# Optimization experiments

Hardware: AMD Instinct MI355X
Metric: run time of the kernel (lower is better)

The kernel has to match this reference:

```python
import jax, jax.numpy as jnp
import numpy as np

D_MODEL = 1024
N_HEADS = 16
D_K = D_MODEL // N_HEADS
B, S = 4, 2048
NEG = -1e9

def setup_inputs() -> dict:
    key = jax.random.key(0)
    ks = jax.random.split(key, 6)
    scale = 1.0 / np.sqrt(D_MODEL)
    x = jax.random.normal(ks[0], (B, S, D_MODEL), dtype=jnp.float32)
    mask = jnp.ones((B, S), dtype=jnp.int32)
    Wq = jax.random.normal(ks[1], (D_MODEL, D_MODEL), dtype=jnp.float32) * scale
    Wk = jax.random.normal(ks[2], (D_MODEL, D_MODEL), dtype=jnp.float32) * scale
    Wv = jax.random.normal(ks[3], (D_MODEL, D_MODEL), dtype=jnp.float32) * scale
    Wo = jax.random.normal(ks[4], (D_MODEL, D_MODEL), dtype=jnp.float32) * scale
    bo = jnp.zeros((D_MODEL,), dtype=jnp.float32)
    return {"x": x, "mask": mask, "Wq": Wq, "Wk": Wk, "Wv": Wv, "Wo": Wo, "bo": bo}

def reference(x, mask, Wq, Wk, Wv, Wo, bo):
    B_, S_ = x.shape[0], x.shape[1]
    # torch nn.Linear: y = x @ W.T
    def proj(W):
        h = jnp.einsum('bsd,ed->bse', x, W)
        return h.reshape(B_, S_, N_HEADS, D_K).transpose(0, 2, 1, 3)  # (B,H,S,Dk)
    Q, K, V = proj(Wq), proj(Wk), proj(Wv)
    scores = jnp.einsum('bhqd,bhkd->bhqk', Q, K) / jnp.sqrt(jnp.float32(D_K))
    causal = jnp.tril(jnp.ones((S_, S_), dtype=bool))  # (S,S)
    scores = jnp.where(causal[None, None], scores, NEG)
    pad = (mask[:, None, None, :] != 0)  # (B,1,1,S) broadcast over keys
    scores = jnp.where(pad, scores, NEG)
    attn = jax.nn.softmax(scores, axis=-1)
    ctx = jnp.einsum('bhqk,bhkd->bhqd', attn, V)
    ctx = ctx.transpose(0, 2, 1, 3).reshape(B_, S_, D_MODEL)
    return jnp.einsum('bsd,ed->bse', ctx, Wo) + bo
```

## Files before the change

### kernel.cpp

```cpp
#include <hip/hip_runtime.h>

typedef unsigned short u16;
typedef unsigned int u32;
typedef unsigned long long u64;
typedef __attribute__((ext_vector_type(8))) u16 u16x8;
typedef __attribute__((ext_vector_type(8))) __bf16 bf16x8;
typedef __attribute__((ext_vector_type(4))) float f32x4;

#define D_MODEL 1024
#define SEQ 2048
#define NBATCH 4
#define NHEAD 16
#define DKH 64

__device__ __forceinline__ u16 f2bf(float f) {
  u32 u = __builtin_bit_cast(u32, f);
  u += 0x7fffu + ((u >> 16) & 1u);
  return (u16)(u >> 16);
}
__device__ __forceinline__ float bf2f(u16 h) {
  u32 u = ((u32)h) << 16;
  return __builtin_bit_cast(float, u);
}
__device__ __forceinline__ f32x4 MFMA(u16x8 a, u16x8 b, f32x4 c) {
  return __builtin_amdgcn_mfma_f32_16x16x32_bf16(
      __builtin_bit_cast(bf16x8, a), __builtin_bit_cast(bf16x8, b), c, 0, 0, 0);
}

#define GLD16(gsrc, ldst)                                                     \
  __builtin_amdgcn_global_load_lds(                                           \
      (const __attribute__((address_space(1))) void*)(gsrc),                  \
      (__attribute__((address_space(3))) void*)(ldst), 16, 0, 0)

__global__ __launch_bounds__(256) void conv_all(
    const float* __restrict__ x, const float* __restrict__ wq,
    const float* __restrict__ wk, const float* __restrict__ wv,
    const float* __restrict__ wo, u16* __restrict__ xb, u16* __restrict__ wqb,
    u16* __restrict__ wkb, u16* __restrict__ wvb, u16* __restrict__ wob) {
  long qd = (long)blockIdx.x * 256 + threadIdx.x;
  long e = qd << 2;
  const float* src;
  u16* dst;
  long off;
  if (e < 8388608L) {
    src = x; dst = xb; off = e;
  } else {
    long j = e - 8388608L;
    int w = (int)(j >> 20);
    off = j & 1048575L;
    src = (w == 0) ? wq : (w == 1) ? wk : (w == 2) ? wv : wo;
    dst = (w == 0) ? wqb : (w == 1) ? wkb : (w == 2) ? wvb : wob;
  }
  float4 v = *(const float4*)(src + off);
  u32 lo32 = (u32)f2bf(v.x) | ((u32)f2bf(v.y) << 16);
  u32 hi32 = (u32)f2bf(v.z) | ((u32)f2bf(v.w) << 16);
  *(u64*)(dst + off) = (u64)lo32 | ((u64)hi32 << 32);
}

template <int MODE>
__global__ __launch_bounds__(256) void gemm_bt(
    const u16* __restrict__ A, const u16* __restrict__ Bm,
    u16* __restrict__ out0, u16* __restrict__ out1, float* __restrict__ Cf,
    const float* __restrict__ bias, int M, int N, int K) {
  __shared__ u16 As[128 * 64];
  __shared__ u16 Bs[128 * 64];
  const int tid = threadIdx.x;
  const int lane = tid & 63, wave = tid >> 6;
  const int lo = lane & 15, g = lane >> 4;
  const int mBase = blockIdx.y * 128, nBase = blockIdx.x * 128;
  const int wr = wave >> 1, wc = wave & 1;

  f32x4 acc[4][4];
#pragma unroll
  for (int mi = 0; mi < 4; ++mi)
#pragma unroll
    for (int ni = 0; ni < 4; ++ni) acc[mi][ni] = (f32x4){0.f, 0.f, 0.f, 0.f};

  const int nK = K >> 6;
  for (int kb = 0; kb < nK; ++kb) {
    __syncthreads();
    const u16* Ab = A + (size_t)mBase * K + kb * 64;
    const u16* Bb = Bm + (size_t)nBase * K + kb * 64;
#pragma unroll
    for (int i = 0; i < 4; ++i) {
      int flat = (i * 256 + tid) * 8;
      int r = flat >> 6, c = flat & 63;
      GLD16(Ab + (size_t)r * K + c, As + (i * 256 + wave * 64) * 8);
    }
#pragma unroll
    for (int i = 0; i < 4; ++i) {
      int flat = (i * 256 + tid) * 8;
      int r = flat >> 6, c = flat & 63;
      GLD16(Bb + (size_t)r * K + c, Bs + (i * 256 + wave * 64) * 8);
    }
    __syncthreads();

#pragma unroll
    for (int kk = 0; kk < 64; kk += 32) {
      u16x8 a[4], b[4];
#pragma unroll
      for (int mi = 0; mi < 4; ++mi)
        a[mi] = *(const u16x8*)&As[(wr * 64 + mi * 16 + lo) * 64 + kk + g * 8];
#pragma unroll
      for (int ni = 0; ni < 4; ++ni)
        b[ni] = *(const u16x8*)&Bs[(wc * 64 + ni * 16 + lo) * 64 + kk + g * 8];
#pragma unroll
      for (int mi = 0; mi < 4; ++mi)
#pragma unroll
        for (int ni = 0; ni < 4; ++ni)
          acc[mi][ni] = MFMA(a[mi], b[ni], acc[mi][ni]);
    }
  }

#pragma unroll
  for (int mi = 0; mi < 4; ++mi)
#pragma unroll
    for (int ni = 0; ni < 4; ++ni) {
      int row0 = mBase + wr * 64 + mi * 16 + g * 4;
      int col = nBase + wc * 64 + ni * 16 + lo;
      float bv = 0.f;
      if constexpr (MODE == 1) bv = bias[col];
#pragma unroll
      for (int r = 0; r < 4; ++r) {
        int row = row0 + r;
        float v = acc[mi][ni][r];
        if constexpr (MODE == 0) {
          out0[(size_t)row * N + col] = f2bf(v);
        } else if constexpr (MODE == 1) {
          Cf[(size_t)row * N + col] = v + bv;
        } else if constexpr (MODE == 2) {
          if (col < 1024) {
            out0[(size_t)row * 1024 + col] = f2bf(v);
          } else {
            int b = row >> 11, s = row & 2047, c = s >> 6, key = s & 63;
            int col2 = col - 1024;
            int h = col2 >> 6, dk = col2 & 63;
            int d16 = dk >> 3, dlo = dk & 7;
            out1[((size_t)((b * 16 + h) * 32 + c)) * 4096 +
                 (key * 8 + (d16 ^ (key & 7))) * 8 + dlo] = f2bf(v);
          }
        } else {
          int h = row >> 6, dk = row & 63;
          int b = col >> 11, s = col & 2047, c = s >> 6, key = s & 63;
          int k16 = key >> 3, klo = key & 7;
          out0[((size_t)((b * 16 + h) * 32 + c)) * 4096 +
               (dk * 8 + (k16 ^ (dk & 7))) * 8 + klo] = f2bf(v);
        }
      }
    }
}

__global__ __launch_bounds__(256) void attn_fwd(
    const u16* __restrict__ Qm, const u16* __restrict__ Kc,
    const u16* __restrict__ Vc, const int* __restrict__ mask,
    u16* __restrict__ ctx) {
  __shared__ u16 Kl[2][4096];
  __shared__ u16 Vl[2][4096];
  __shared__ u16 Plds[4][16 * 72];
  const int bid0 = blockIdx.x;
  const int xcd = bid0 & 7, gi = (bid0 >> 3) & 7, tz = bid0 >> 6;
  const int t = 31 - tz;
  const int gh = xcd * 8 + gi;
  const int h = gh & 15, b = gh >> 4;
  const int q0 = t << 6;
  const int tid = threadIdx.x;
  const int lane = tid & 63, wave = tid >> 6;
  const int lo = lane & 15, g = lane >> 4;
  char* P = (char*)&Plds[wave][0];

  const int qrow = q0 + wave * 16 + lo;

  const size_t qoff = ((size_t)(b * SEQ + qrow)) * 1024 + h * DKH + g * 8;
  u16x8 bq0 = *(const u16x8*)(Qm + qoff);
  u16x8 bq1 = *(const u16x8*)(Qm + qoff + 32);
#pragma unroll
  for (int j = 0; j < 8; ++j) {
    bq0[j] = (u16)(__builtin_bit_cast(u32, bf2f(bq0[j]) * 0.125f) >> 16);
    bq1[j] = (u16)(__builtin_bit_cast(u32, bf2f(bq1[j]) * 0.125f) >> 16);
  }

  const u16* KcB = Kc + (size_t)gh * 131072;
  const u16* VcB = Vc + (size_t)gh * 131072;

#define STAGE(bufi, cc)                                                       \
  {                                                                           \
    const u16* kp_ = KcB + (size_t)(cc)*4096;                                 \
    const u16* vp_ = VcB + (size_t)(cc)*4096;                                 \
    GLD16(kp_ + tid * 8, &Kl[bufi][wave * 512]);                              \
    GLD16(kp_ + 2048 + tid * 8, &Kl[bufi][2048 + wave * 512]);                \
    GLD16(vp_ + tid * 8, &Vl[bufi][wave * 512]);                              \
    GLD16(vp_ + 2048 + tid * 8, &Vl[bufi][2048 + wave * 512]);                \
  }

  float m = -1e9f, lsum = 0.f;
  f32x4 o[4];
#pragma unroll
  for (int dt = 0; dt < 4; ++dt) o[dt] = (f32x4){0.f, 0.f, 0.f, 0.f};

  int cur = 0;
  STAGE(0, 0);
  int mv = mask[b * SEQ + lane];

#pragma unroll 1
  for (int c = 0; c <= t; ++c) {
    __syncthreads();
    if (c < t) STAGE(cur ^ 1, c + 1);

    u64 bm = __ballot(mv != 0);

    u16x8 ak0[4], ak1[4];
#pragma unroll
    for (int kt = 0; kt < 4; ++kt) {
      int key = kt * 16 + lo, sw = key & 7;
      ak0[kt] = *(const u16x8*)&Kl[cur][(key * 8 + (g ^ sw)) * 8];
      ak1[kt] = *(const u16x8*)&Kl[cur][(key * 8 + ((4 + g) ^ sw)) * 8];
    }

    f32x4 s[4];
#pragma unroll
    for (int kt = 0; kt < 4; ++kt) {
      f32x4 z = (f32x4){0.f, 0.f, 0.f, 0.f};
      s[kt] = MFMA(ak0[kt], bq0, z);
      s[kt] = MFMA(ak1[kt], bq1, s[kt]);
    }

    const int cn = (c < t) ? c + 1 : t;
    mv = mask[b * SEQ + (cn << 6) + lane];

    if (bm != ~0ull || c == t) {
#pragma unroll
      for (int kt = 0; kt < 4; ++kt)
#pragma unroll
        for (int r = 0; r < 4; ++r) {
          int kl = kt * 16 + g * 4 + r;
          int kk = (c << 6) + kl;
          if ((kk > qrow) || (((bm >> kl) & 1ull) == 0)) s[kt][r] = -1e9f;
        }
    }

    float c0 = fmaxf(fmaxf(s[0][0], s[0][1]), fmaxf(s[0][2], s[0][3]));
    float c1 = fmaxf(fmaxf(s[1][0], s[1][1]), fmaxf(s[1][2], s[1][3]));
    float c2 = fmaxf(fmaxf(s[2][0], s[2][1]), fmaxf(s[2][2], s[2][3]));
    float c3 = fmaxf(fmaxf(s[3][0], s[3][1]), fmaxf(s[3][2], s[3][3]));
    float cm = fmaxf(fmaxf(c0, c1), fmaxf(c2, c3));
    cm = fmaxf(cm, __shfl_xor(cm, 16));
    cm = fmaxf(cm, __shfl_xor(cm, 32));
    float mn = fmaxf(m, cm);
    float fsc = __expf(m - mn);
    m = mn;

    float rsk[4];
#pragma unroll
    for (int kt = 0; kt < 4; ++kt) {
      float p0 = __expf(s[kt][0] - mn);
      float p1 = __expf(s[kt][1] - mn);
      float p2 = __expf(s[kt][2] - mn);
      float p3 = __expf(s[kt][3] - mn);
      rsk[kt] = (p0 + p1) + (p2 + p3);
      u32 w0 = (u32)f2bf(p0) | ((u32)f2bf(p1) << 16);
      u32 w1 = (u32)f2bf(p2) | ((u32)f2bf(p3) << 16);
      int key = kt * 16 + g * 4;
      int byteoff =
          lo * 144 + ((((key >> 3) ^ (lo & 7)) << 4) | ((key & 7) << 1));
      *(u64*)(P + byteoff) = (u64)w0 | ((u64)w1 << 32);
    }

    float rs = (rsk[0] + rsk[1]) + (rsk[2] + rsk[3]);
    rs += __shfl_xor(rs, 16);
    rs += __shfl_xor(rs, 32);
    lsum = lsum * fsc + rs;

#pragma unroll
    for (int r = 0; r < 4; ++r) {
      float fr = __shfl(fsc, (g << 2) + r);
      o[0][r] *= fr;
      o[1][r] *= fr;
      o[2][r] *= fr;
      o[3][r] *= fr;
    }

    u16x8 ap0 = *(const u16x8*)(P + lo * 144 + ((g ^ (lo & 7)) << 4));
    u16x8 ap1 = *(const u16x8*)(P + lo * 144 + (((4 + g) ^ (lo & 7)) << 4));
#pragma unroll
    for (int dt = 0; dt < 4; ++dt) {
      int dk = dt * 16 + lo, sw = dk & 7;
      u16x8 bv0 = *(const u16x8*)&Vl[cur][(dk * 8 + (g ^ sw)) * 8];
      u16x8 bv1 = *(const u16x8*)&Vl[cur][(dk * 8 + ((4 + g) ^ sw)) * 8];
      o[dt] = MFMA(ap0, bv0, o[dt]);
      o[dt] = MFMA(ap1, bv1, o[dt]);
    }

    cur ^= 1;
  }

#pragma unroll
  for (int r = 0; r < 4; ++r) {
    float lr = __shfl(lsum, (g << 2) + r);
    float inv = 1.f / lr;
    int row = q0 + wave * 16 + (g << 2) + r;
#pragma unroll
    for (int dt = 0; dt < 4; ++dt) {
      int col = h * DKH + dt * 16 + lo;
      ctx[((size_t)(b * SEQ + row)) * D_MODEL + col] = f2bf(o[dt][r] * inv);
    }
  }
}

extern "C" void kernel_launch(void* const* d_in, const int* in_sizes, int n_in,
                              void* d_out, int out_size, void* d_ws,
                              size_t ws_size, hipStream_t stream) {
  const float* x = (const float*)d_in[0];
  const int* mask = (const int*)d_in[1];
  const float* Wq = (const float*)d_in[2];
  const float* Wk = (const float*)d_in[3];
  const float* Wv = (const float*)d_in[4];
  const float* Wo = (const float*)d_in[5];
  const float* bo = (const float*)d_in[6];
  float* out = (float*)d_out;

  u16* xb = (u16*)d_ws;
  u16* wqb = xb + 8388608;
  u16* wkb = wqb + 1048576;
  u16* wvb = wkb + 1048576;
  u16* wob = wvb + 1048576;
  u16* Qm = wob + 1048576;
  u16* Kc = Qm + 8388608;
  u16* Vc = Kc + 8388608;
  u16* ctx = Vc + 8388608;
  if (ws_size < (size_t)46137344 * 2) return;

  conv_all<<<12288, 256, 0, stream>>>(x, Wq, Wk, Wv, Wo, xb, wqb, wkb, wvb, wob);

  gemm_bt<2><<<dim3(16, 64), 256, 0, stream>>>(xb, wqb, Qm, Kc, nullptr,
                                               nullptr, 8192, 2048, 1024);
  gemm_bt<3><<<dim3(64, 8), 256, 0, stream>>>(wvb, xb, Vc, nullptr, nullptr,
                                              nullptr, 1024, 8192, 1024);

  attn_fwd<<<2048, 256, 0, stream>>>(Qm, Kc, Vc, mask, ctx);

  gemm_bt<1><<<dim3(8, 64), 256, 0, stream>>>(ctx, wob, nullptr, nullptr, out,
                                              bo, 8192, 1024, 1024);
}
```

Measured before the change: 316.6 us.

## Fuse QKV projections into one GEMM and defer softmax rescaling in attention

```diff
diff --git a/kernel.cpp b/kernel.cpp
--- a/kernel.cpp
+++ b/kernel.cpp
@@ -1,4 +1,5 @@
 #include <hip/hip_runtime.h>
+#include <math.h>
 
 typedef unsigned short u16;
 typedef unsigned int u32;
@@ -22,6 +23,8 @@
   u32 u = ((u32)h) << 16;
   return __builtin_bit_cast(float, u);
 }
+__device__ __forceinline__ float E2(float x) { return exp2f(x); }
+
 __device__ __forceinline__ f32x4 MFMA(u16x8 a, u16x8 b, f32x4 c) {
   return __builtin_amdgcn_mfma_f32_16x16x32_bf16(
       __builtin_bit_cast(bf16x8, a), __builtin_bit_cast(bf16x8, b), c, 0, 0, 0);
@@ -60,8 +63,9 @@
 template <int MODE>
 __global__ __launch_bounds__(256) void gemm_bt(
     const u16* __restrict__ A, const u16* __restrict__ Bm,
-    u16* __restrict__ out0, u16* __restrict__ out1, float* __restrict__ Cf,
-    const float* __restrict__ bias, int M, int N, int K) {
+    u16* __restrict__ out0, u16* __restrict__ out1, u16* __restrict__ out2,
+    float* __restrict__ Cf, const float* __restrict__ bias, int M, int N,
+    int K) {
   __shared__ u16 As[128 * 64];
   __shared__ u16 Bs[128 * 64];
   const int tid = threadIdx.x;
@@ -128,23 +132,24 @@
           out0[(size_t)row * N + col] = f2bf(v);
         } else if constexpr (MODE == 1) {
           Cf[(size_t)row * N + col] = v + bv;
-        } else if constexpr (MODE == 2) {
+        } else {
           if (col < 1024) {
             out0[(size_t)row * 1024 + col] = f2bf(v);
+          } else if (col < 2048) {
+            int bb = row >> 11, s = row & 2047, cc = s >> 6, key = s & 63;
+            int col2 = col - 1024;
+            int hh = col2 >> 6, dk = col2 & 63;
+            int d16 = dk >> 3, dlo = dk & 7;
+            out1[((size_t)((bb * 16 + hh) * 32 + cc)) * 4096 +
+                 (key * 8 + (d16 ^ (key & 7))) * 8 + dlo] = f2bf(v);
           } else {
-            int b = row >> 11, s = row & 2047, c = s >> 6, key = s & 63;
-            int col2 = col - 1024;
-            int h = col2 >> 6, dk = col2 & 63;
-            int d16 = dk >> 3, dlo = dk & 7;
-            out1[((size_t)((b * 16 + h) * 32 + c)) * 4096 +
-                 (key * 8 + (d16 ^ (key & 7))) * 8 + dlo] = f2bf(v);
+            int bb = row >> 11, s = row & 2047, cc = s >> 6, key = s & 63;
+            int col2 = col - 2048;
+            int hh = col2 >> 6, dk = col2 & 63;
+            int k16 = key >> 3, klo = key & 7;
+            out2[((size_t)((bb * 16 + hh) * 32 + cc)) * 4096 +
+                 (dk * 8 + (k16 ^ (dk & 7))) * 8 + klo] = f2bf(v);
           }
-        } else {
-          int h = row >> 6, dk = row & 63;
-          int b = col >> 11, s = col & 2047, c = s >> 6, key = s & 63;
-          int k16 = key >> 3, klo = key & 7;
-          out0[((size_t)((b * 16 + h) * 32 + c)) * 4096 +
-               (dk * 8 + (k16 ^ (dk & 7))) * 8 + klo] = f2bf(v);
         }
       }
     }
@@ -156,7 +161,7 @@
     u16* __restrict__ ctx) {
   __shared__ u16 Kl[2][4096];
   __shared__ u16 Vl[2][4096];
-  __shared__ u16 Plds[4][16 * 72];
+  __shared__ u16 Plds[4][16 * 64];
   const int bid0 = blockIdx.x;
   const int xcd = bid0 & 7, gi = (bid0 >> 3) & 7, tz = bid0 >> 6;
   const int t = 31 - tz;
@@ -170,13 +175,14 @@
 
   const int qrow = q0 + wave * 16 + lo;
 
+  const float SCL = 0.125f * 1.44269504f;
   const size_t qoff = ((size_t)(b * SEQ + qrow)) * 1024 + h * DKH + g * 8;
   u16x8 bq0 = *(const u16x8*)(Qm + qoff);
   u16x8 bq1 = *(const u16x8*)(Qm + qoff + 32);
 #pragma unroll
   for (int j = 0; j < 8; ++j) {
-    bq0[j] = (u16)(__builtin_bit_cast(u32, bf2f(bq0[j]) * 0.125f) >> 16);
-    bq1[j] = (u16)(__builtin_bit_cast(u32, bf2f(bq1[j]) * 0.125f) >> 16);
+    bq0[j] = f2bf(bf2f(bq0[j]) * SCL);
+    bq1[j] = f2bf(bf2f(bq1[j]) * SCL);
   }
 
   const u16* KcB = Kc + (size_t)gh * 131072;
@@ -245,42 +251,46 @@
     float cm = fmaxf(fmaxf(c0, c1), fmaxf(c2, c3));
     cm = fmaxf(cm, __shfl_xor(cm, 16));
     cm = fmaxf(cm, __shfl_xor(cm, 32));
-    float mn = fmaxf(m, cm);
-    float fsc = __expf(m - mn);
-    m = mn;
+    const bool defer = (__all(cm <= m + 8.0f) != 0);
+    const float mn = defer ? m : fmaxf(m, cm);
 
     float rsk[4];
 #pragma unroll
     for (int kt = 0; kt < 4; ++kt) {
-      float p0 = __expf(s[kt][0] - mn);
-      float p1 = __expf(s[kt][1] - mn);
-      float p2 = __expf(s[kt][2] - mn);
-      float p3 = __expf(s[kt][3] - mn);
+      float p0 = E2(s[kt][0] - mn);
+      float p1 = E2(s[kt][1] - mn);
+      float p2 = E2(s[kt][2] - mn);
+      float p3 = E2(s[kt][3] - mn);
       rsk[kt] = (p0 + p1) + (p2 + p3);
       u32 w0 = (u32)f2bf(p0) | ((u32)f2bf(p1) << 16);
       u32 w1 = (u32)f2bf(p2) | ((u32)f2bf(p3) << 16);
       int key = kt * 16 + g * 4;
       int byteoff =
-          lo * 144 + ((((key >> 3) ^ (lo & 7)) << 4) | ((key & 7) << 1));
+          lo * 128 + ((((key >> 3) ^ (lo & 7)) << 4) | ((key & 7) << 1));
       *(u64*)(P + byteoff) = (u64)w0 | ((u64)w1 << 32);
     }
 
     float rs = (rsk[0] + rsk[1]) + (rsk[2] + rsk[3]);
     rs += __shfl_xor(rs, 16);
     rs += __shfl_xor(rs, 32);
-    lsum = lsum * fsc + rs;
-
-#pragma unroll
-    for (int r = 0; r < 4; ++r) {
-      float fr = __shfl(fsc, (g << 2) + r);
-      o[0][r] *= fr;
-      o[1][r] *= fr;
-      o[2][r] *= fr;
-      o[3][r] *= fr;
-    }
-
-    u16x8 ap0 = *(const u16x8*)(P + lo * 144 + ((g ^ (lo & 7)) << 4));
-    u16x8 ap1 = *(const u16x8*)(P + lo * 144 + (((4 + g) ^ (lo & 7)) << 4));
+    if (defer) {
+      lsum += rs;
+    } else {
+      float fsc = E2(m - mn);
+      lsum = lsum * fsc + rs;
+      m = mn;
+#pragma unroll
+      for (int r = 0; r < 4; ++r) {
+        float fr = __shfl(fsc, (g << 2) + r);
+        o[0][r] *= fr;
+        o[1][r] *= fr;
+        o[2][r] *= fr;
+        o[3][r] *= fr;
+      }
+    }
+
+    u16x8 ap0 = *(const u16x8*)(P + lo * 128 + ((g ^ (lo & 7)) << 4));
+    u16x8 ap1 = *(const u16x8*)(P + lo * 128 + (((4 + g) ^ (lo & 7)) << 4));
 #pragma unroll
     for (int dt = 0; dt < 4; ++dt) {
       int dk = dt * 16 + lo, sw = dk & 7;
@@ -331,13 +341,12 @@
 
   conv_all<<<12288, 256, 0, stream>>>(x, Wq, Wk, Wv, Wo, xb, wqb, wkb, wvb, wob);
 
-  gemm_bt<2><<<dim3(16, 64), 256, 0, stream>>>(xb, wqb, Qm, Kc, nullptr,
-                                               nullptr, 8192, 2048, 1024);
-  gemm_bt<3><<<dim3(64, 8), 256, 0, stream>>>(wvb, xb, Vc, nullptr, nullptr,
-                                              nullptr, 1024, 8192, 1024);
+  gemm_bt<4><<<dim3(24, 64), 256, 0, stream>>>(xb, wqb, Qm, Kc, Vc, nullptr,
+                                               nullptr, 8192, 3072, 1024);
 
   attn_fwd<<<2048, 256, 0, stream>>>(Qm, Kc, Vc, mask, ctx);
 
-  gemm_bt<1><<<dim3(8, 64), 256, 0, stream>>>(ctx, wob, nullptr, nullptr, out,
-                                              bo, 8192, 1024, 1024);
-}
+  gemm_bt<1><<<dim3(8, 64), 256, 0, stream>>>(ctx, wob, nullptr, nullptr,
+                                              nullptr, out, bo, 8192, 1024,
+                                              1024);
+}
```

Measured after the change: 299.4 us. 1.06x faster.
